# Kernel tuning notes

Hardware: AMD Instinct MI355X
Metric: run time of the kernel (lower is better)

The kernel has to match this reference:

```python
import jax, jax.numpy as jnp
import numpy as np
import math

B, D, H, DK = 24, 64, 8, 8
N, M, CN = 256, 64, 16
VW, VC, CE, WE = 30000, 128, 200, 300

FREQS = jnp.asarray(np.array([10000.0 ** (-i / D) if i % 2 == 0 else -(10000.0 ** (-(i - 1) / D)) for i in range(D)], dtype=np.float32)[:, None])
PHASES = jnp.asarray(np.array([0.0 if i % 2 == 0 else math.pi / 2 for i in range(D)], dtype=np.float32)[:, None])

def _norm(x, eps=1e-6):
    mu = x.mean(-1, keepdims=True)
    var = ((x - mu) ** 2).sum(-1, keepdims=True) / (x.shape[-1] - 1)  # torch std is unbiased
    return (x - mu) / (jnp.sqrt(var) + eps)

def _pos_enc(x):
    pos = jnp.arange(x.shape[-1], dtype=x.dtype)[None, :]
    return jnp.sin(jnp.sin(pos * FREQS + PHASES)) + x  # double sin kept faithful to source

def _conv1d(x, w, groups=1, pad=0, b=None):
    y = jax.lax.conv_general_dilated(x, w, (1,), [(pad, pad)], dimension_numbers=('NCH', 'OIH', 'NCH'), feature_group_count=groups)
    return y if b is None else y + b[None, :, None]

def _dwsep1d(x, dw, pw, db=None, pb=None):
    y = _conv1d(x, dw, groups=x.shape[1], pad=dw.shape[-1] // 2, b=db)
    return _conv1d(y, pw, b=pb)

def _conv2d(x, w, groups=1, pad=0, b=None):
    y = jax.lax.conv_general_dilated(x, w, (1, 1), [(pad, pad), (pad, pad)], dimension_numbers=('NCHW', 'OIHW', 'NCHW'), feature_group_count=groups)
    return y if b is None else y + b[None, :, None, None]

def _highway(x, lw, lb, gw, gb):
    x = x.transpose(0, 2, 1)  # [B,L,D]
    for i in range(lw.shape[0]):
        g = jax.nn.sigmoid(jnp.einsum('bld,od->blo', x, gw[i]) + gb[i])
        nl = jax.nn.relu(jnp.einsum('bld,od->blo', x, lw[i]) + lb[i])
        x = g * nl + (1.0 - g) * x
    return x.transpose(0, 2, 1)

def _embed(ch, wd, e2dw, e2db, e2pw, e2pb, e1dw, e1db, e1pw, e1pb, hlw, hlb, hgw, hgb):
    ch = ch.transpose(0, 3, 1, 2)  # [B,CE,L,CN]
    ch = _conv2d(ch, e2dw, groups=CE, pad=2, b=e2db)
    ch = _conv2d(ch, e2pw, b=e2pb)
    ch = jax.nn.relu(ch).max(axis=3)  # [B,D,L]
    wd = wd.transpose(0, 2, 1)  # [B,WE,L]
    emb = jnp.concatenate([ch, wd], axis=1)
    emb = _dwsep1d(emb, e1dw, e1pw, e1db, e1pb)
    return _highway(emb, hlw, hlb, hgw, hgb)

def _self_att(x, wq, wk, wv, wo):
    Qh = jnp.einsum('hbkd,bdl->hbkl', wq, x)
    Kh = jnp.einsum('hbkd,bdl->hbkl', wk, x)
    Vh = jnp.einsum('hbkd,bdl->hbkl', wv, x)
    scores = jnp.einsum('hbkl,hbkm->hblm', Qh, Kh) / math.sqrt(DK)
    att = jax.nn.softmax(scores, axis=2)  # torch softmax dim=1 over [B,l,m]
    head = jnp.einsum('hbvl,hblm->hbvm', Vh, att)
    head = head.transpose(1, 0, 2, 3).reshape(B, H * DK, x.shape[-1])
    return jnp.einsum('bod,bdl->bol', wo, head)

def _enc_block(x, dw, pw, wq, wk, wv, wo, W):
    out = _pos_enc(x)
    res = out
    for i in range(dw.shape[0]):
        out = jax.nn.relu(_dwsep1d(_norm(out), dw[i], pw[i]))
        out = res + out
        res = out  # dropout is a no-op in this deterministic reference
    out = res + _self_att(_norm(out), wq, wk, wv, wo)
    res = out
    out = jax.nn.relu(jnp.einsum('bod,bdl->bol', W, _norm(out)))
    return res + out

def _cq_att(C, Q, W):
    # S[b,i,j] = W . [Q[:,j]; C[:,i]; Q[:,j]*C[:,i]] -- vectorized trilinear similarity
    wq, wc, wm = W[:, 0, :D], W[:, 0, D:2 * D], W[:, 0, 2 * D:]
    S = (jnp.einsum('bd,bdn->bn', wc, C)[:, :, None]
         + jnp.einsum('bd,bdm->bm', wq, Q)[:, None, :]
         + jnp.einsum('bdn,bdm->bnm', C * wm[:, :, None], Q))
    S1 = jax.nn.softmax(S, axis=2)
    S2 = jax.nn.softmax(S, axis=1)
    A = jnp.einsum('bdm,bnm->bdn', Q, S1)
    X = jnp.einsum('bnm,bkm->bnk', S1, S2)  # S1 @ S2^T
    Bm = jnp.einsum('bdn,bkn->bdk', C, X)   # C @ X^T
    return jnp.concatenate([C, A, C * A, C * Bm], axis=1)

def _pointer(M0, M1, M2, w0, w1):
    Y0 = jnp.einsum('bd,bdn->bn', w0[:, 0], jnp.concatenate([M0, M1], axis=1))
    Y1 = jnp.einsum('bd,bdn->bn', w1[:, 0], jnp.concatenate([M0, M2], axis=1))
    return jax.nn.softmax(Y0, axis=1), jax.nn.softmax(Y1, axis=1)  # exp(log_softmax)

def _qanet(flt, Cwid, Ccid, Qwid, Qcid):
    (word_table, char_table,
     e2dw, e2db, e2pw, e2pb, e1dw, e1db, e1pw, e1pb,
     hlw, hlb, hgw, hgb,
     ce_dw, ce_pw, ce_wq, ce_wk, ce_wv, ce_wo, ce_w,
     qe_dw, qe_pw, qe_wq, qe_wk, qe_wv, qe_wo, qe_w,
     m0_dw, m0_pw, m0_wq, m0_wk, m0_wv, m0_wo, m0_w,
     m1_dw, m1_pw, m1_wq, m1_wk, m1_wv, m1_wo, m1_w,
     m2_dw, m2_pw, m2_wq, m2_wk, m2_wv, m2_wo, m2_w,
     cq_w, rs_dw, rs_pw, p_w0, p_w1) = flt
    emb_p = (e2dw, e2db, e2pw, e2pb, e1dw, e1db, e1pw, e1pb, hlw, hlb, hgw, hgb)
    C = _embed(char_table[Ccid], word_table[Cwid], *emb_p)
    Q = _embed(char_table[Qcid], word_table[Qwid], *emb_p)
    C = _enc_block(C, ce_dw, ce_pw, ce_wq, ce_wk, ce_wv, ce_wo, ce_w)
    Q = _enc_block(Q, qe_dw, qe_pw, qe_wq, qe_wk, qe_wv, qe_wo, qe_w)
    X = _cq_att(C, Q, cq_w)
    X = _dwsep1d(X, rs_dw, rs_pw)
    M0 = X
    for _ in range(7):
        M0 = _enc_block(M0, m0_dw, m0_pw, m0_wq, m0_wk, m0_wv, m0_wo, m0_w)
    M1 = M0
    for _ in range(7):
        M1 = _enc_block(M1, m1_dw, m1_pw, m1_wq, m1_wk, m1_wv, m1_wo, m1_w)
    M2 = M1
    for _ in range(7):
        M2 = _enc_block(M2, m2_dw, m2_pw, m2_wq, m2_wk, m2_wv, m2_wo, m2_w)
    return _pointer(M0, M1, M2, p_w0, p_w1)

def setup_inputs() -> dict:
    key = jax.random.key(0)
    ks = iter(jax.random.split(key, 80))
    rn = lambda shape, s=0.1: jax.random.normal(next(ks), shape, jnp.float32) * s
    inp = {}
    inp['word_table'] = rn((VW, WE), 1.0)
    inp['char_table'] = rn((VC, CE), 1.0)
    inp['e2dw'] = rn((CE, 1, 5, 5)); inp['e2db'] = jnp.zeros((CE,), jnp.float32)
    inp['e2pw'] = rn((D, CE, 1, 1)); inp['e2pb'] = jnp.zeros((D,), jnp.float32)
    inp['e1dw'] = rn((WE + D, 1, 5)); inp['e1db'] = jnp.zeros((WE + D,), jnp.float32)
    inp['e1pw'] = rn((D, WE + D, 1)); inp['e1pb'] = jnp.zeros((D,), jnp.float32)
    inp['hlw'] = rn((2, D, D)); inp['hlb'] = jnp.zeros((2, D), jnp.float32)
    inp['hgw'] = rn((2, D, D)); inp['hgb'] = jnp.zeros((2, D), jnp.float32)
    for p, (cnum, k_) in [('ce', (4, 7)), ('qe', (4, 7)), ('m0', (2, 5)), ('m1', (2, 5)), ('m2', (2, 5))]:
        inp[p + '_dw'] = rn((cnum, D, 1, k_))
        inp[p + '_pw'] = rn((cnum, D, D, 1))
        inp[p + '_wq'] = rn((H, B, DK, D))
        inp[p + '_wk'] = rn((H, B, DK, D))
        inp[p + '_wv'] = rn((H, B, DK, D))
        inp[p + '_wo'] = rn((B, D, D))
        inp[p + '_w'] = rn((B, D, D))
    inp['cq_w'] = rn((B, 1, 3 * D))
    inp['rs_dw'] = rn((4 * D, 1, 5))
    inp['rs_pw'] = rn((D, 4 * D, 1))
    inp['p_w0'] = rn((B, 1, 2 * D))
    inp['p_w1'] = rn((B, 1, 2 * D))
    inp['Cwid'] = jax.random.randint(next(ks), (B, N), 0, VW)
    inp['Ccid'] = jax.random.randint(next(ks), (B, N, CN), 0, VC)
    inp['Qwid'] = jax.random.randint(next(ks), (B, M), 0, VW)
    inp['Qcid'] = jax.random.randint(next(ks), (B, M, CN), 0, VC)
    return inp

def reference(word_table, char_table, e2dw, e2db, e2pw, e2pb, e1dw, e1db, e1pw, e1pb, hlw, hlb, hgw, hgb, ce_dw, ce_pw, ce_wq, ce_wk, ce_wv, ce_wo, ce_w, qe_dw, qe_pw, qe_wq, qe_wk, qe_wv, qe_wo, qe_w, m0_dw, m0_pw, m0_wq, m0_wk, m0_wv, m0_wo, m0_w, m1_dw, m1_pw, m1_wq, m1_wk, m1_wv, m1_wo, m1_w, m2_dw, m2_pw, m2_wq, m2_wk, m2_wv, m2_wo, m2_w, cq_w, rs_dw, rs_pw, p_w0, p_w1, Cwid, Ccid, Qwid, Qcid):
    flt = (word_table, char_table, e2dw, e2db, e2pw, e2pb, e1dw, e1db, e1pw, e1pb, hlw, hlb, hgw, hgb, ce_dw, ce_pw, ce_wq, ce_wk, ce_wv, ce_wo, ce_w, qe_dw, qe_pw, qe_wq, qe_wk, qe_wv, qe_wo, qe_w, m0_dw, m0_pw, m0_wq, m0_wk, m0_wv, m0_wo, m0_w, m1_dw, m1_pw, m1_wq, m1_wk, m1_wv, m1_wo, m1_w, m2_dw, m2_pw, m2_wq, m2_wk, m2_wv, m2_wo, m2_w, cq_w, rs_dw, rs_pw, p_w0, p_w1)
    p0, p1 = _qanet(flt, Cwid, Ccid, Qwid, Qcid)
    return p0, p1
```

## Files before the change

### kernel.cpp

```cpp
#include <hip/hip_runtime.h>
#include <math.h>

constexpr int B = 24, HH = 8;
constexpr int NN = 256, MQ = 64;
constexpr int EC = 364;

#define PI_2 1.5707963267948966f

__device__ __forceinline__ void combine_stats(const float* __restrict__ parts,
                                              int row, int NT, float Lf,
                                              float& mu, float& inv) {
  float s = 0.f, q = 0.f;
  for (int t = 0; t < NT; ++t) {
    s += parts[((size_t)row * 4 + t) * 2];
    q += parts[((size_t)row * 4 + t) * 2 + 1];
  }
  mu = s / Lf;
  float var = (q - s * mu) / (Lf - 1.f);
  if (var < 0.f) var = 0.f;
  inv = 1.f / (sqrtf(var) + 1e-6f);
}

__global__ void k_prep(float* __restrict__ tab,
                       const float* __restrict__ e2pw, const float* __restrict__ e1pw,
                       const float* __restrict__ hlw, const float* __restrict__ hgw,
                       const float* __restrict__ e2dw,
                       float* __restrict__ pwT, float* __restrict__ e1pwT,
                       float* __restrict__ hlwT, float* __restrict__ hgwT,
                       float* __restrict__ dwT) {
  int blk = blockIdx.x;
  if (blk < 64) {
    int d = blk, l = threadIdx.x;
    float fr = ((d & 1) == 0) ? powf(10000.f, -(float)d / 64.f)
                              : -powf(10000.f, -(float)(d - 1) / 64.f);
    float ph = (d & 1) ? PI_2 : 0.f;
    tab[d * 256 + l] = sinf(sinf((float)l * fr + ph));
    return;
  }
  int i = (blk - 64) * 256 + threadIdx.x;
  if (i < 12800) {
    int ce = i >> 6, o = i & 63;
    pwT[i] = e2pw[o * 200 + ce];
    return;
  }
  i -= 12800;
  if (i < 23296) {
    int c = i >> 6, o = i & 63;
    e1pwT[i] = e1pw[o * EC + c];
    return;
  }
  i -= 23296;
  if (i < 8192) {
    int layer = i >> 12, rem = i & 4095;
    int d = rem >> 6, o = rem & 63;
    hlwT[i] = hlw[layer * 4096 + o * 64 + d];
    return;
  }
  i -= 8192;
  if (i < 8192) {
    int layer = i >> 12, rem = i & 4095;
    int d = rem >> 6, o = rem & 63;
    hgwT[i] = hgw[layer * 4096 + o * 64 + d];
    return;
  }
  i -= 8192;
  if (i < 5000) {
    int t = i / 200, ce = i % 200;
    dwT[i] = e2dw[ce * 25 + t];
  }
}

template<bool COPY>
__global__ void k_posadd_stats(float* __restrict__ XC, const float* __restrict__ srcC,
                               float* __restrict__ XQ, const float* __restrict__ tab,
                               float* __restrict__ partsC, float* __restrict__ partsQ) {
  int which = blockIdx.y;
  float* X = which ? XQ : XC;
  float* parts = which ? partsQ : partsC;
  int L = which ? 64 : 256;
  int row = blockIdx.x * 4 + (threadIdx.x >> 6);
  int lane = threadIdx.x & 63;
  int d = row & 63;
  float* xr = X + (size_t)row * L;
  const float* sr = (COPY && !which) ? (srcC + (size_t)row * L) : xr;
  int NT = L >> 6;
  for (int t = 0; t < NT; ++t) {
    int l = t * 64 + lane;
    float v = sr[l] + tab[d * 256 + l];
    xr[l] = v;
    float s = v, q = v * v;
#pragma unroll
    for (int o = 32; o > 0; o >>= 1) { s += __shfl_xor(s, o); q += __shfl_xor(q, o); }
    if (lane == 0) {
      parts[((size_t)row * 4 + t) * 2] = s;
      parts[((size_t)row * 4 + t) * 2 + 1] = q;
    }
  }
}

template<int K>
__global__ __launch_bounds__(512) void k_fconv(
    const float* __restrict__ XiC, float* __restrict__ XoC,
    const float* __restrict__ XiQ, float* __restrict__ XoQ,
    const float* __restrict__ dwC, const float* __restrict__ pwC,
    const float* __restrict__ dwQ, const float* __restrict__ pwQ,
    const float* __restrict__ pinC, float* __restrict__ poutC,
    const float* __restrict__ pinQ, float* __restrict__ poutQ) {
  constexpr int H = K / 2, SW = 64 + 2 * H;
  __shared__ float smu[64], sinv[64];
  __shared__ float sN[64 * SW];
  __shared__ float sD[64 * 65];
  __shared__ __align__(16) float sWt[4096];
  int b = blockIdx.x, t = blockIdx.y;
  const float *Xin, *dw, *pw, *pin; float *Xout, *pout; int L, tile;
  if (t < 4) { Xin = XiC; Xout = XoC; dw = dwC; pw = pwC; pin = pinC; pout = poutC; L = 256; tile = t; }
  else       { Xin = XiQ; Xout = XoQ; dw = dwQ; pw = pwQ; pin = pinQ; pout = poutQ; L = 64;  tile = 0; }
  int lt = tile * 64;
  int tid = threadIdx.x;
  int NT = L >> 6;
  if (tid < 64) combine_stats(pin, b * 64 + tid, NT, (float)L, smu[tid], sinv[tid]);
  for (int i = tid; i < 1024; i += 512)
    ((float4*)sWt)[i] = ((const float4*)pw)[i];
  const float* Xb = Xin + (size_t)b * 64 * L;
  int l = tid & 63, og = tid >> 6;
  float rres[8];
#pragma unroll
  for (int j = 0; j < 8; ++j)
    rres[j] = Xb[(size_t)(og * 8 + j) * L + lt + l];
  __syncthreads();
  for (int i = tid; i < 64 * SW; i += 512) {
    int c = i / SW, jj = i % SW;
    int gl = lt + jj - H;
    sN[i] = (gl >= 0 && gl < L) ? (Xb[(size_t)c * L + gl] - smu[c]) * sinv[c] : 0.f;
  }
  __syncthreads();
  for (int i = tid; i < 4096; i += 512) {
    int c = i >> 6, ll = i & 63;
    float acc = 0.f;
#pragma unroll
    for (int k = 0; k < K; ++k) acc += sN[c * SW + ll + k] * dw[c * K + k];
    sD[c * 65 + ll] = acc;
  }
  __syncthreads();
  float acc[8];
#pragma unroll
  for (int j = 0; j < 8; ++j) acc[j] = 0.f;
  for (int c = 0; c < 64; ++c) {
    float av = sD[c * 65 + l];
#pragma unroll
    for (int j = 0; j < 8; ++j) acc[j] += sWt[(og * 8 + j) * 64 + c] * av;
  }
  __syncthreads();
  float* Ob = Xout + (size_t)b * 64 * L;
#pragma unroll
  for (int j = 0; j < 8; ++j) {
    int o = og * 8 + j;
    float v = rres[j] + fmaxf(acc[j], 0.f);
    Ob[(size_t)o * L + lt + l] = v;
    sD[o * 65 + l] = v;
  }
  __syncthreads();
  if (tid < 64) {
    int o = tid;
    float s = 0.f, q = 0.f;
    for (int l2 = 0; l2 < 64; ++l2) { float v = sD[o * 65 + l2]; s += v; q += v * v; }
    pout[((size_t)(b * 64 + o) * 4 + tile) * 2] = s;
    pout[((size_t)(b * 64 + o) * 4 + tile) * 2 + 1] = q;
  }
}

template<bool NORM, bool RELU, bool STATS, bool ADDTAB>
__global__ __launch_bounds__(512) void k_matmul2(
    const float* __restrict__ AC, const float* __restrict__ WC,
    const float* __restrict__ resC, float* __restrict__ outC2,
    const float* __restrict__ pinC, float* __restrict__ poutC,
    const float* __restrict__ AQ, const float* __restrict__ WQ,
    const float* __restrict__ resQ, float* __restrict__ outQ2,
    const float* __restrict__ pinQ, float* __restrict__ poutQ,
    const float* __restrict__ tab) {
  __shared__ float sA[64 * 65];
  __shared__ __align__(16) float sW[4096];
  __shared__ float smu[64], sinv[64];
  int b = blockIdx.x, t = blockIdx.y;
  const float *A, *W, *res, *pin; float *outp, *pout; int L, tile;
  if (t < 4) { A = AC; W = WC; res = resC; outp = outC2; pin = pinC; pout = poutC; L = 256; tile = t; }
  else       { A = AQ; W = WQ; res = resQ; outp = outQ2; pin = pinQ; pout = poutQ; L = 64;  tile = 0; }
  int lt = tile * 64;
  int tid = threadIdx.x;
  int NT = L >> 6;
  if (NORM && tid < 64) combine_stats(pin, b * 64 + tid, NT, (float)L, smu[tid], sinv[tid]);
  const float* Wb = W + (size_t)b * 4096;
  for (int i = tid; i < 1024; i += 512)
    ((float4*)sW)[i] = ((const float4*)Wb)[i];
  int l = tid & 63, og = tid >> 6;
  float rres[8], rtab[8];
#pragma unroll
  for (int j = 0; j < 8; ++j) {
    int o = og * 8 + j;
    rres[j] = res[((size_t)b * 64 + o) * L + lt + l];
    if (ADDTAB) rtab[j] = tab[o * 256 + lt + l];
  }
  if (NORM) __syncthreads();
  const float* Ab = A + (size_t)b * 64 * L;
  for (int i = tid; i < 1024; i += 512) {
    int c = i >> 4, lq = (i & 15) * 4;
    float4 v = *(const float4*)(Ab + (size_t)c * L + lt + lq);
    if (NORM) {
      float mu = smu[c], iv = sinv[c];
      v.x = (v.x - mu) * iv; v.y = (v.y - mu) * iv;
      v.z = (v.z - mu) * iv; v.w = (v.w - mu) * iv;
    }
    sA[c * 65 + lq] = v.x; sA[c * 65 + lq + 1] = v.y;
    sA[c * 65 + lq + 2] = v.z; sA[c * 65 + lq + 3] = v.w;
  }
  __syncthreads();
  float acc[8];
#pragma unroll
  for (int j = 0; j < 8; ++j) acc[j] = 0.f;
  for (int c = 0; c < 64; ++c) {
    float av = sA[c * 65 + l];
#pragma unroll
    for (int j = 0; j < 8; ++j) acc[j] += sW[(og * 8 + j) * 64 + c] * av;
  }
  if (STATS) __syncthreads();
#pragma unroll
  for (int j = 0; j < 8; ++j) {
    int o = og * 8 + j;
    float v = acc[j];
    if (RELU) v = fmaxf(v, 0.f);
    v += rres[j];
    if (ADDTAB) v += rtab[j];
    outp[((size_t)b * 64 + o) * L + lt + l] = v;
    if (STATS) sA[o * 65 + l] = v;
  }
  if (STATS) {
    __syncthreads();
    if (tid < 64) {
      int o = tid;
      float s = 0.f, q = 0.f;
      for (int l2 = 0; l2 < 64; ++l2) { float v = sA[o * 65 + l2]; s += v; q += v * v; }
      pout[((size_t)(b * 64 + o) * 4 + tile) * 2] = s;
      pout[((size_t)(b * 64 + o) * 4 + tile) * 2 + 1] = q;
    }
  }
}

__global__ __launch_bounds__(256) void k_resize(
    const float* __restrict__ Xcat, const float* __restrict__ dw,
    const float* __restrict__ pw, float* __restrict__ out) {
  __shared__ float sA[64 * 64];
  int b = blockIdx.x, lt = blockIdx.y * 64;
  int l = threadIdx.x & 63, og = threadIdx.x >> 6;
  float acc[16];
#pragma unroll
  for (int j = 0; j < 16; ++j) acc[j] = 0.f;
  for (int c0 = 0; c0 < 256; c0 += 64) {
    __syncthreads();
    for (int i = threadIdx.x; i < 4096; i += 256) {
      int c = (i >> 6) + c0, ll = (i & 63) + lt;
      const float* xr = Xcat + ((size_t)b * 256 + c) * 256;
      float a = 0.f;
#pragma unroll
      for (int k = 0; k < 5; ++k) {
        int p = ll + k - 2;
        if (p >= 0 && p < 256) a += xr[p] * dw[c * 5 + k];
      }
      sA[i] = a;
    }
    __syncthreads();
    for (int c = 0; c < 64; ++c) {
      float av = sA[c * 64 + l];
#pragma unroll
      for (int j = 0; j < 16; ++j)
        acc[j] += pw[(size_t)(og * 16 + j) * 256 + c0 + c] * av;
    }
  }
#pragma unroll
  for (int j = 0; j < 16; ++j)
    out[((size_t)b * 64 + og * 16 + j) * 256 + lt + l] = acc[j];
}

__global__ __launch_bounds__(512) void k_att(
    const float* __restrict__ XC, const float* __restrict__ partsC,
    const float* __restrict__ wqC, const float* __restrict__ wkC,
    const float* __restrict__ wvC, float* __restrict__ hcC,
    const float* __restrict__ XQ, const float* __restrict__ partsQ,
    const float* __restrict__ wqQ, const float* __restrict__ wkQ,
    const float* __restrict__ wvQ, float* __restrict__ hcQ) {
  int h = blockIdx.x, b2 = blockIdx.y;
  const float *X, *parts, *wq, *wk, *wv; float* hc; int L, b;
  if (b2 < B) { X = XC; parts = partsC; wq = wqC; wk = wkC; wv = wvC; hc = hcC; L = 256; b = b2; }
  else        { X = XQ; parts = partsQ; wq = wqQ; wk = wkQ; wv = wvQ; hc = hcQ; L = 64;  b = b2 - B; }
  __shared__ float smu[64], sinv[64];
  __shared__ float sX[64 * 65];
  __shared__ float sQ[2048], sK8[2048], sV[2048];
  __shared__ float swq[512], swk[512], swv[512];
  int tid = threadIdx.x;
  int NT = L >> 6;
  if (tid < 64) combine_stats(parts, b * 64 + tid, NT, (float)L, smu[tid], sinv[tid]);
  size_t woff = (size_t)(h * B + b) * 512;
  swq[tid] = wq[woff + tid];
  swk[tid] = wk[woff + tid];
  swv[tid] = wv[woff + tid];
  __syncthreads();
  const float* Xb = X + (size_t)b * 64 * L;
  for (int lt = 0; lt < L; lt += 64) {
    for (int i = tid; i < 4096; i += 512) {
      int d = i >> 6, l = i & 63;
      sX[d * 65 + l] = (Xb[(size_t)d * L + lt + l] - smu[d]) * sinv[d];
    }
    __syncthreads();
    {
      int k = tid >> 6, l = tid & 63;
      float aq = 0.f, ak = 0.f, av = 0.f;
      for (int d = 0; d < 64; ++d) {
        float x = sX[d * 65 + l];
        aq += swq[k * 64 + d] * x;
        ak += swk[k * 64 + d] * x;
        av += swv[k * 64 + d] * x;
      }
      sQ[k * L + lt + l] = aq; sK8[k * L + lt + l] = ak; sV[k * L + lt + l] = av;
    }
    __syncthreads();
  }
  const float scale = 0.35355339059327373f;
  int m = tid & 255, half = tid >> 8;
  int L2 = L >> 1;
  float mx = -1e30f, sum = 0.f, acc[8];
#pragma unroll
  for (int v = 0; v < 8; ++v) acc[v] = 0.f;
  if (m < L) {
    float kc[8];
#pragma unroll
    for (int k = 0; k < 8; ++k) kc[k] = sK8[k * L + m];
    int l0 = half * L2, l1 = l0 + L2;
    for (int l = l0; l < l1; ++l) {
      float s = 0.f;
#pragma unroll
      for (int k = 0; k < 8; ++k) s += sQ[k * L + l] * kc[k];
      s *= scale;
      if (s <= mx) {
        float p = __expf(s - mx);
        sum += p;
#pragma unroll
        for (int v = 0; v < 8; ++v) acc[v] += p * sV[v * L + l];
      } else {
        float corr = __expf(mx - s);
        sum = sum * corr + 1.f;
#pragma unroll
        for (int v = 0; v < 8; ++v) acc[v] = acc[v] * corr + sV[v * L + l];
        mx = s;
      }
    }
  }
  swq[tid] = mx;
  swk[tid] = sum;
  float* pacc = sX;
#pragma unroll
  for (int v = 0; v < 8; ++v) pacc[tid * 8 + v] = acc[v];
  __syncthreads();
  if (half == 0 && m < L) {
    float m0 = swq[m], m1 = swq[256 + m];
    float mT = fmaxf(m0, m1);
    float c0 = __expf(m0 - mT), c1 = __expf(m1 - mT);
    float s = swk[m] * c0 + swk[256 + m] * c1;
    float is = 1.f / s;
#pragma unroll
    for (int v = 0; v < 8; ++v) {
      float a = pacc[m * 8 + v] * c0 + pacc[(256 + m) * 8 + v] * c1;
      hc[((size_t)b * 64 + h * 8 + v) * L + m] = a * is;
    }
  }
}

__global__ __launch_bounds__(256) void k_charembed(
    const int* __restrict__ cidC, const int* __restrict__ cidQ,
    const float* __restrict__ ctab, const float* __restrict__ dwT,
    const float* __restrict__ db, const float* __restrict__ pwT,
    const float* __restrict__ pb,
    float* __restrict__ outC, float* __restrict__ outQ) {
  int nx = blockIdx.x, b = blockIdx.y;
  const int* cid; float* out; int Ln, n;
  if (nx < NN) { cid = cidC; out = outC; Ln = NN; n = nx; }
  else         { cid = cidQ; out = outQ; Ln = MQ; n = nx - NN; }
  __shared__ float dwo[16 * 200];
  __shared__ int sid[5][16];
  __shared__ float red[256];
  int tid = threadIdx.x;
  if (tid < 80) {
    int kn = tid / 16, cn = tid % 16;
    int nn = n + kn - 2;
    sid[kn][cn] = (nn >= 0 && nn < Ln) ? cid[((size_t)b * Ln + nn) * 16 + cn] : -1;
  }
  __syncthreads();
  for (int i = tid; i < 16 * 200; i += 256) {
    int cn = i / 200, ce = i % 200;
    float r[25];
#pragma unroll
    for (int kn = 0; kn < 5; ++kn) {
#pragma unroll
      for (int kc = 0; kc < 5; ++kc) {
        int cc = cn + kc - 2;
        int id = (cc >= 0 && cc < 16) ? sid[kn][cc] : -1;
        r[kn * 5 + kc] = (id >= 0) ? ctab[(size_t)id * 200 + ce] : 0.f;
      }
    }
    float acc = db[ce];
#pragma unroll
    for (int t = 0; t < 25; ++t) acc += r[t] * dwT[t * 200 + ce];
    dwo[cn * 200 + ce] = acc;
  }
  __syncthreads();
  int o = tid & 63, q = tid >> 6;
  float acc4[4];
#pragma unroll
  for (int k = 0; k < 4; ++k) acc4[k] = pb[o];
  for (int c0 = 0; c0 < 200; c0 += 8) {
    float w8[8];
#pragma unroll
    for (int j = 0; j < 8; ++j) w8[j] = pwT[(c0 + j) * 64 + o];
#pragma unroll
    for (int k = 0; k < 4; ++k) {
      const float* dr = dwo + (q + k * 4) * 200 + c0;
#pragma unroll
      for (int j = 0; j < 8; ++j) acc4[k] += w8[j] * dr[j];
    }
  }
  float mx = -1e30f;
#pragma unroll
  for (int k = 0; k < 4; ++k) mx = fmaxf(mx, acc4[k]);
  red[tid] = mx;
  __syncthreads();
  if (q == 0) {
    mx = fmaxf(fmaxf(red[o], red[64 + o]), fmaxf(red[128 + o], red[192 + o]));
    out[((size_t)b * 64 + o) * Ln + n] = fmaxf(mx, 0.f);
  }
}

__global__ void k_embhw(const float* __restrict__ chxC, const float* __restrict__ chxQ,
                        const int* __restrict__ widC, const int* __restrict__ widQ,
                        const float* __restrict__ wtab, const float* __restrict__ dw,
                        const float* __restrict__ db, const float* __restrict__ pwT,
                        const float* __restrict__ pb,
                        const float* __restrict__ lwT, const float* __restrict__ lb,
                        const float* __restrict__ gwT, const float* __restrict__ gb,
                        float* __restrict__ outC, float* __restrict__ outQ) {
  int nx = blockIdx.x, b = blockIdx.y;
  const float* chx; const int* wid; float* out; int Ln, n;
  if (nx < NN) { chx = chxC; wid = widC; out = outC; Ln = NN; n = nx; }
  else         { chx = chxQ; wid = widQ; out = outQ; Ln = MQ; n = nx - NN; }
  __shared__ float dwc[EC];
  __shared__ int sw[5];
  __shared__ float x[64], xn[64];
  int tid = threadIdx.x;
  if (tid < 5) {
    int nn = n + tid - 2;
    sw[tid] = (nn >= 0 && nn < Ln) ? wid[(size_t)b * Ln + nn] : -1;
  }
  __syncthreads();
  for (int ch = tid; ch < EC; ch += 64) {
    float r[5];
#pragma unroll
    for (int k = 0; k < 5; ++k) {
      int nn = n + k - 2;
      float v = 0.f;
      if (nn >= 0 && nn < Ln) {
        if (ch < 64) v = chx[((size_t)b * 64 + ch) * Ln + nn];
        else v = wtab[(size_t)sw[k] * 300 + (ch - 64)];
      }
      r[k] = v;
    }
    float acc = db[ch];
#pragma unroll
    for (int k = 0; k < 5; ++k) acc += r[k] * dw[ch * 5 + k];
    dwc[ch] = acc;
  }
  __syncthreads();
  int o = tid;
  float acc = pb[o];
  for (int c0 = 0; c0 < EC; c0 += 4) {
    float w4[4];
#pragma unroll
    for (int j = 0; j < 4; ++j) w4[j] = pwT[(c0 + j) * 64 + o];
#pragma unroll
    for (int j = 0; j < 4; ++j) acc += w4[j] * dwc[c0 + j];
  }
  x[o] = acc;
  __syncthreads();
  for (int layer = 0; layer < 2; ++layer) {
    const float* lwr = lwT + layer * 4096;
    const float* gwr = gwT + layer * 4096;
    float gl = gb[layer * 64 + o], nl = lb[layer * 64 + o];
    for (int d0 = 0; d0 < 64; d0 += 8) {
      float g8[8], l8[8];
#pragma unroll
      for (int j = 0; j < 8; ++j) { g8[j] = gwr[(d0 + j) * 64 + o]; l8[j] = lwr[(d0 + j) * 64 + o]; }
#pragma unroll
      for (int j = 0; j < 8; ++j) { gl += g8[j] * x[d0 + j]; nl += l8[j] * x[d0 + j]; }
    }
    float g = 1.f / (1.f + __expf(-gl));
    float r = fmaxf(nl, 0.f);
    xn[o] = g * r + (1.f - g) * x[o];
    __syncthreads();
    x[o] = xn[o];
    __syncthreads();
  }
  out[((size_t)b * 64 + o) * Ln + n] = x[o];
}

__global__ __launch_bounds__(256) void k_cqS(const float* __restrict__ C,
                                             const float* __restrict__ Q,
                                             const float* __restrict__ w,
                                             float* __restrict__ S,
                                             float* __restrict__ rmax,
                                             float* __restrict__ rsum) {
  int b = blockIdx.x, nt = blockIdx.y * 64;
  __shared__ float sQ[4096], sC[4096], ct[64], qt[64], swb[192];
  const float* Cb = C + (size_t)b * 64 * 256;
  const float* Qb = Q + (size_t)b * 4096;
  const float* wb = w + (size_t)b * 192;
  if (threadIdx.x < 192) swb[threadIdx.x] = wb[threadIdx.x];
  for (int i = threadIdx.x; i < 4096; i += 256) {
    int d = i >> 6, m = i & 63;
    sQ[i] = Qb[d * 64 + m];
    sC[i] = Cb[d * 256 + nt + m];
  }
  __syncthreads();
  if (threadIdx.x < 64) {
    int j = threadIdx.x;
    float a = 0.f, c2 = 0.f;
    for (int d = 0; d < 64; ++d) {
      a += swb[64 + d] * sC[d * 64 + j];
      c2 += swb[d] * sQ[d * 64 + j];
    }
    ct[j] = a; qt[j] = c2;
  }
  __syncthreads();
  int m = threadIdx.x & 63, wv = threadIdx.x >> 6;
  for (int it = 0; it < 16; ++it) {
    int nl = wv + it * 4;
    float acc = ct[nl] + qt[m];
    for (int d = 0; d < 64; ++d)
      acc += sC[d * 64 + nl] * swb[128 + d] * sQ[d * 64 + m];
    S[((size_t)b * 256 + nt + nl) * 64 + m] = acc;
    float mx = acc;
#pragma unroll
    for (int o = 32; o > 0; o >>= 1) mx = fmaxf(mx, __shfl_xor(mx, o));
    float p = __expf(acc - mx);
#pragma unroll
    for (int o = 32; o > 0; o >>= 1) p += __shfl_xor(p, o);
    if (m == 0) { rmax[b * 256 + nt + nl] = mx; rsum[b * 256 + nt + nl] = p; }
  }
}

__global__ void k_cqcol(const float* __restrict__ S, float* __restrict__ cmax,
                        float* __restrict__ csum) {
  int b = blockIdx.x, m = threadIdx.x;
  const float* Sb = S + (size_t)b * 256 * 64;
  float mx = -1e30f;
  for (int n = 0; n < 256; ++n) mx = fmaxf(mx, Sb[n * 64 + m]);
  float s = 0.f;
  for (int n = 0; n < 256; ++n) s += __expf(Sb[n * 64 + m] - mx);
  cmax[b * 64 + m] = mx; csum[b * 64 + m] = s;
}

__global__ __launch_bounds__(256) void k_cqA_CS2(
    const float* __restrict__ C, const float* __restrict__ Q,
    const float* __restrict__ S, const float* __restrict__ rmax,
    const float* __restrict__ rsum, const float* __restrict__ cmax,
    const float* __restrict__ csum, float* __restrict__ Xcat,
    float* __restrict__ CS2) {
  __shared__ float sh[8256];
  int b = blockIdx.x, t = blockIdx.y;
  int tid = threadIdx.x;
  if (t < 4) {
    float* sQ = sh; float* sP = sh + 4096;
    int nt = t * 64;
    const float* Qb = Q + (size_t)b * 4096;
    for (int i = tid; i < 4096; i += 256) sQ[i] = Qb[i];
    for (int i = tid; i < 4096; i += 256) {
      int nl = i >> 6, m = i & 63;
      int n = nt + nl;
      sP[nl * 65 + m] = __expf(S[((size_t)b * 256 + n) * 64 + m] - rmax[b * 256 + n]) / rsum[b * 256 + n];
    }
    __syncthreads();
    int nl = tid & 63, dg = tid >> 6;
    int n = nt + nl;
    for (int j = 0; j < 16; ++j) {
      int d = dg * 16 + j;
      float acc = 0.f;
      for (int m = 0; m < 64; ++m) acc += sQ[d * 64 + m] * sP[nl * 65 + m];
      float cv = C[((size_t)b * 64 + d) * 256 + n];
      Xcat[((size_t)b * 256 + d) * 256 + n] = cv;
      Xcat[((size_t)b * 256 + 64 + d) * 256 + n] = acc;
      Xcat[((size_t)b * 256 + 128 + d) * 256 + n] = cv * acc;
    }
  } else {
    float* sP = sh; float* sC = sh + 4096;
    int m = tid & 63, dg = tid >> 6;
    float acc[16];
#pragma unroll
    for (int j = 0; j < 16; ++j) acc[j] = 0.f;
    for (int nt = 0; nt < 4; ++nt) {
      __syncthreads();
      for (int i = tid; i < 4096; i += 256) {
        int nl = i >> 6, mm = i & 63;
        int n = nt * 64 + nl;
        sP[i] = __expf(S[((size_t)b * 256 + n) * 64 + mm] - cmax[b * 64 + mm]) / csum[b * 64 + mm];
        int d = i >> 6, nn = i & 63;
        sC[i] = C[((size_t)b * 64 + d) * 256 + nt * 64 + nn];
      }
      __syncthreads();
      for (int nl = 0; nl < 64; ++nl) {
        float p = sP[nl * 64 + m];
#pragma unroll
        for (int j = 0; j < 16; ++j) acc[j] += sC[(dg * 16 + j) * 64 + nl] * p;
      }
    }
    for (int j = 0; j < 16; ++j)
      CS2[((size_t)b * 64 + dg * 16 + j) * 64 + m] = acc[j];
  }
}

__global__ __launch_bounds__(256) void k_cqBm(
    const float* __restrict__ C, const float* __restrict__ CS2,
    const float* __restrict__ S, const float* __restrict__ rmax,
    const float* __restrict__ rsum, float* __restrict__ Xcat) {
  int b = blockIdx.x, kt = blockIdx.y * 64;
  __shared__ float sW[4096];
  __shared__ float sP[64 * 65];
  for (int i = threadIdx.x; i < 4096; i += 256) sW[i] = CS2[(size_t)b * 4096 + i];
  for (int i = threadIdx.x; i < 4096; i += 256) {
    int kl = i >> 6, m = i & 63;
    int k = kt + kl;
    sP[kl * 65 + m] = __expf(S[((size_t)b * 256 + k) * 64 + m] - rmax[b * 256 + k]) / rsum[b * 256 + k];
  }
  __syncthreads();
  int kl = threadIdx.x & 63, dg = threadIdx.x >> 6;
  int k = kt + kl;
  for (int j = 0; j < 16; ++j) {
    int d = dg * 16 + j;
    float acc = 0.f;
    for (int m = 0; m < 64; ++m) acc += sW[d * 64 + m] * sP[kl * 65 + m];
    float cv = C[((size_t)b * 64 + d) * 256 + k];
    Xcat[((size_t)b * 256 + 192 + d) * 256 + k] = cv * acc;
  }
}

__global__ void k_pointer2(const float* __restrict__ M0, const float* __restrict__ M1,
                           const float* __restrict__ M2, const float* __restrict__ w0,
                           const float* __restrict__ w1, float* __restrict__ out) {
  int b = blockIdx.x, sel = blockIdx.y, n = threadIdx.x;
  const float* wb = (sel ? w1 : w0) + b * 128;
  const float* Mb = sel ? M2 : M1;
  float y = 0.f;
  for (int d = 0; d < 64; ++d) {
    y += wb[d] * M0[((size_t)b * 64 + d) * 256 + n];
    y += wb[64 + d] * Mb[((size_t)b * 64 + d) * 256 + n];
  }
  __shared__ float wred[4], wsum[4];
  int lane = n & 63, wid = n >> 6;
  float mx = y;
#pragma unroll
  for (int o = 32; o > 0; o >>= 1) mx = fmaxf(mx, __shfl_xor(mx, o));
  if (lane == 0) wred[wid] = mx;
  __syncthreads();
  mx = fmaxf(fmaxf(wred[0], wred[1]), fmaxf(wred[2], wred[3]));
  float e = __expf(y - mx);
  float s = e;
#pragma unroll
  for (int o = 32; o > 0; o >>= 1) s += __shfl_xor(s, o);
  if (lane == 0) wsum[wid] = s;
  __syncthreads();
  s = wsum[0] + wsum[1] + wsum[2] + wsum[3];
  out[sel * 6144 + b * 256 + n] = e / s;
}

extern "C" void kernel_launch(void* const* d_in, const int* in_sizes, int n_in,
                              void* d_out, int out_size, void* d_ws, size_t ws_size,
                              hipStream_t stream) {
  const float* word_table = (const float*)d_in[0];
  const float* char_table = (const float*)d_in[1];
  const float* e2dw = (const float*)d_in[2];
  const float* e2db = (const float*)d_in[3];
  const float* e2pw = (const float*)d_in[4];
  const float* e2pb = (const float*)d_in[5];
  const float* e1dw = (const float*)d_in[6];
  const float* e1db = (const float*)d_in[7];
  const float* e1pw = (const float*)d_in[8];
  const float* e1pb = (const float*)d_in[9];
  const float* hlw = (const float*)d_in[10];
  const float* hlb = (const float*)d_in[11];
  const float* hgw = (const float*)d_in[12];
  const float* hgb = (const float*)d_in[13];
  const float *enc_dw[5], *enc_pw[5], *enc_wq[5], *enc_wk[5], *enc_wv[5], *enc_wo[5], *enc_w[5];
  for (int p = 0; p < 5; ++p) {
    enc_dw[p] = (const float*)d_in[14 + 7 * p + 0];
    enc_pw[p] = (const float*)d_in[14 + 7 * p + 1];
    enc_wq[p] = (const float*)d_in[14 + 7 * p + 2];
    enc_wk[p] = (const float*)d_in[14 + 7 * p + 3];
    enc_wv[p] = (const float*)d_in[14 + 7 * p + 4];
    enc_wo[p] = (const float*)d_in[14 + 7 * p + 5];
    enc_w[p]  = (const float*)d_in[14 + 7 * p + 6];
  }
  const float* cq_w  = (const float*)d_in[49];
  const float* rs_dw = (const float*)d_in[50];
  const float* rs_pw = (const float*)d_in[51];
  const float* p_w0  = (const float*)d_in[52];
  const float* p_w1  = (const float*)d_in[53];
  const int* Cwid = (const int*)d_in[54];
  const int* Ccid = (const int*)d_in[55];
  const int* Qwid = (const int*)d_in[56];
  const int* Qcid = (const int*)d_in[57];
  float* out = (float*)d_out;

  float* ws = (float*)d_ws;
  float* postab = ws;
  float* U    = ws + 16384;
  float* Xcat = ws + 409600;
  float* CX   = ws + 1982464;
  float* Sb   = ws + 2375680;
  float* QX   = ws + 2768896;
  float* CS2  = ws + 2867200;
  float* rmax = ws + 2965504;
  float* rsum = ws + 2971648;
  float* cmax = ws + 2977792;
  float* csum = ws + 2979328;
  float* P0   = ws + 2980864;
  float* P1   = ws + 2993152;
  float* pwT  = ws + 3005440;
  float* e1pwT= ws + 3018240;
  float* hlwT = ws + 3041536;
  float* hgwT = ws + 3049728;
  float* dwT  = ws + 3057920;
  float* P0Q  = ws + 3062920;
  float* P1Q  = ws + 3075208;
  float* UQ   = ws + 3087496;
  float* M0 = CX; float* M1 = Sb; float* M2 = Xcat;
  float* E1C = Xcat;
  float* E1Q = Xcat + 393216;
  (void)out_size; (void)in_sizes; (void)n_in; (void)ws_size;

  auto run_enc = [&](float* X, const float* src, int p, int reps) {
    if (src)
      hipLaunchKernelGGL((k_posadd_stats<true>), dim3(384, 1), dim3(256), 0, stream,
                         X, src, (float*)nullptr, postab, P0, (float*)nullptr);
    else
      hipLaunchKernelGGL((k_posadd_stats<false>), dim3(384, 1), dim3(256), 0, stream,
                         X, (const float*)nullptr, (float*)nullptr, postab, P0, (float*)nullptr);
    for (int rep = 0; rep < reps; ++rep) {
      float* pin = P0; float* pout = P1;
      float* Xi = X; float* Xo = U;
      for (int i = 0; i < 2; ++i) {
        hipLaunchKernelGGL((k_fconv<5>), dim3(B, 4), dim3(512), 0, stream,
                           (const float*)Xi, Xo, (const float*)nullptr, (float*)nullptr,
                           enc_dw[p] + i * 64 * 5, enc_pw[p] + (size_t)i * 4096,
                           (const float*)nullptr, (const float*)nullptr,
                           pin, pout, (const float*)nullptr, (float*)nullptr);
        { float* t = pin; pin = pout; pout = t; }
        { float* t = Xi; Xi = Xo; Xo = t; }
      }
      k_att<<<dim3(HH, B), 512, 0, stream>>>(X, pin, enc_wq[p], enc_wk[p], enc_wv[p], U,
                                             (const float*)nullptr, (const float*)nullptr,
                                             (const float*)nullptr, (const float*)nullptr,
                                             (const float*)nullptr, (float*)nullptr);
      hipLaunchKernelGGL((k_matmul2<false, false, true, false>), dim3(B, 4), dim3(512), 0, stream,
                         (const float*)U, enc_wo[p], (const float*)X, X, (const float*)nullptr, pout,
                         (const float*)nullptr, (const float*)nullptr, (const float*)nullptr,
                         (float*)nullptr, (const float*)nullptr, (float*)nullptr,
                         (const float*)nullptr);
      if (rep + 1 < reps)
        hipLaunchKernelGGL((k_matmul2<true, true, true, true>), dim3(B, 4), dim3(512), 0, stream,
                           (const float*)X, enc_w[p], (const float*)X, X, pout, P0,
                           (const float*)nullptr, (const float*)nullptr, (const float*)nullptr,
                           (float*)nullptr, (const float*)nullptr, (float*)nullptr,
                           (const float*)postab);
      else
        hipLaunchKernelGGL((k_matmul2<true, true, false, false>), dim3(B, 4), dim3(512), 0, stream,
                           (const float*)X, enc_w[p], (const float*)X, X, pout, (float*)nullptr,
                           (const float*)nullptr, (const float*)nullptr, (const float*)nullptr,
                           (float*)nullptr, (const float*)nullptr, (float*)nullptr,
                           (const float*)nullptr);
    }
  };

  k_prep<<<289, 256, 0, stream>>>(postab, e2pw, e1pw, hlw, hgw, e2dw,
                                  pwT, e1pwT, hlwT, hgwT, dwT);
  k_charembed<<<dim3(NN + MQ, B), 256, 0, stream>>>(Ccid, Qcid, char_table, dwT, e2db, pwT, e2pb, E1C, E1Q);
  k_embhw<<<dim3(NN + MQ, B), 64, 0, stream>>>(E1C, E1Q, Cwid, Qwid, word_table, e1dw, e1db,
                                               e1pwT, e1pb, hlwT, hlb, hgwT, hgb, CX, QX);
  {
    hipLaunchKernelGGL((k_posadd_stats<false>), dim3(384, 2), dim3(256), 0, stream,
                       CX, (const float*)nullptr, QX, postab, P0, P0Q);
    float *pinC = P0, *poutC = P1, *pinQ = P0Q, *poutQ = P1Q;
    float *XiC = CX, *XoC = U, *XiQ = QX, *XoQ = UQ;
    for (int i = 0; i < 4; ++i) {
      hipLaunchKernelGGL((k_fconv<7>), dim3(B, 5), dim3(512), 0, stream,
                         (const float*)XiC, XoC, (const float*)XiQ, XoQ,
                         enc_dw[0] + i * 64 * 7, enc_pw[0] + (size_t)i * 4096,
                         enc_dw[1] + i * 64 * 7, enc_pw[1] + (size_t)i * 4096,
                         pinC, poutC, pinQ, poutQ);
      { float* t = pinC; pinC = poutC; poutC = t; }
      { float* t = pinQ; pinQ = poutQ; poutQ = t; }
      { float* t = XiC; XiC = XoC; XoC = t; }
      { float* t = XiQ; XiQ = XoQ; XoQ = t; }
    }
    k_att<<<dim3(HH, 2 * B), 512, 0, stream>>>(CX, pinC, enc_wq[0], enc_wk[0], enc_wv[0], U,
                                               QX, pinQ, enc_wq[1], enc_wk[1], enc_wv[1], UQ);
    hipLaunchKernelGGL((k_matmul2<false, false, true, false>), dim3(B, 5), dim3(512), 0, stream,
                       (const float*)U, enc_wo[0], (const float*)CX, CX, (const float*)nullptr, poutC,
                       (const float*)UQ, enc_wo[1], (const float*)QX, QX, (const float*)nullptr, poutQ,
                       (const float*)nullptr);
    hipLaunchKernelGGL((k_matmul2<true, true, false, false>), dim3(B, 5), dim3(512), 0, stream,
                       (const float*)CX, enc_w[0], (const float*)CX, CX, poutC, (float*)nullptr,
                       (const float*)QX, enc_w[1], (const float*)QX, QX, poutQ, (float*)nullptr,
                       (const float*)nullptr);
  }
  k_cqS<<<dim3(B, 4), 256, 0, stream>>>(CX, QX, cq_w, Sb, rmax, rsum);
  k_cqcol<<<B, 64, 0, stream>>>(Sb, cmax, csum);
  k_cqA_CS2<<<dim3(B, 5), 256, 0, stream>>>(CX, QX, Sb, rmax, rsum, cmax, csum, Xcat, CS2);
  k_cqBm<<<dim3(B, 4), 256, 0, stream>>>(CX, CS2, Sb, rmax, rsum, Xcat);
  k_resize<<<dim3(B, 4), 256, 0, stream>>>(Xcat, rs_dw, rs_pw, M0);
  run_enc(M0, nullptr, 2, 7);
  run_enc(M1, M0, 3, 7);
  run_enc(M2, M1, 4, 7);
  k_pointer2<<<dim3(B, 2), 256, 0, stream>>>(M0, M1, M2, p_w0, p_w1, out);
}
```

Before: 2.431 ms.

## Fuse model-encoder posadd/stats into producers and use 1024-thread conv/matmul blocks

Removes the separate k_posadd_stats launches before each model encoder pass. The resize kernel now adds the positional table and writes row statistics itself, and the last FFN matmul of each encoder writes both its output and the next encoder's table-added input with stats (DUAL mode). Separately, the fconv and matmul2 kernels go from 512 to 1024 threads with 4 outputs per thread instead of 8. This raises parallelism within each block but halves per-thread register reuse of the shared-memory activation loads.

```diff
diff --git a/kernel.cpp b/kernel.cpp
--- a/kernel.cpp
+++ b/kernel.cpp
@@ -70,9 +70,8 @@
   }
 }
 
-template<bool COPY>
-__global__ void k_posadd_stats(float* __restrict__ XC, const float* __restrict__ srcC,
-                               float* __restrict__ XQ, const float* __restrict__ tab,
+__global__ void k_posadd_stats(float* __restrict__ XC, float* __restrict__ XQ,
+                               const float* __restrict__ tab,
                                float* __restrict__ partsC, float* __restrict__ partsQ) {
   int which = blockIdx.y;
   float* X = which ? XQ : XC;
@@ -82,11 +81,10 @@
   int lane = threadIdx.x & 63;
   int d = row & 63;
   float* xr = X + (size_t)row * L;
-  const float* sr = (COPY && !which) ? (srcC + (size_t)row * L) : xr;
   int NT = L >> 6;
   for (int t = 0; t < NT; ++t) {
     int l = t * 64 + lane;
-    float v = sr[l] + tab[d * 256 + l];
+    float v = xr[l] + tab[d * 256 + l];
     xr[l] = v;
     float s = v, q = v * v;
 #pragma unroll
@@ -99,7 +97,7 @@
 }
 
 template<int K>
-__global__ __launch_bounds__(512) void k_fconv(
+__global__ __launch_bounds__(1024) void k_fconv(
     const float* __restrict__ XiC, float* __restrict__ XoC,
     const float* __restrict__ XiQ, float* __restrict__ XoQ,
     const float* __restrict__ dwC, const float* __restrict__ pwC,
@@ -119,22 +117,22 @@
   int tid = threadIdx.x;
   int NT = L >> 6;
   if (tid < 64) combine_stats(pin, b * 64 + tid, NT, (float)L, smu[tid], sinv[tid]);
-  for (int i = tid; i < 1024; i += 512)
+  for (int i = tid; i < 1024; i += 1024)
     ((float4*)sWt)[i] = ((const float4*)pw)[i];
   const float* Xb = Xin + (size_t)b * 64 * L;
   int l = tid & 63, og = tid >> 6;
-  float rres[8];
-#pragma unroll
-  for (int j = 0; j < 8; ++j)
-    rres[j] = Xb[(size_t)(og * 8 + j) * L + lt + l];
-  __syncthreads();
-  for (int i = tid; i < 64 * SW; i += 512) {
+  float rres[4];
+#pragma unroll
+  for (int j = 0; j < 4; ++j)
+    rres[j] = Xb[(size_t)(og * 4 + j) * L + lt + l];
+  __syncthreads();
+  for (int i = tid; i < 64 * SW; i += 1024) {
     int c = i / SW, jj = i % SW;
     int gl = lt + jj - H;
     sN[i] = (gl >= 0 && gl < L) ? (Xb[(size_t)c * L + gl] - smu[c]) * sinv[c] : 0.f;
   }
   __syncthreads();
-  for (int i = tid; i < 4096; i += 512) {
+  for (int i = tid; i < 4096; i += 1024) {
     int c = i >> 6, ll = i & 63;
     float acc = 0.f;
 #pragma unroll
@@ -142,19 +140,19 @@
     sD[c * 65 + ll] = acc;
   }
   __syncthreads();
-  float acc[8];
-#pragma unroll
-  for (int j = 0; j < 8; ++j) acc[j] = 0.f;
+  float acc[4];
+#pragma unroll
+  for (int j = 0; j < 4; ++j) acc[j] = 0.f;
   for (int c = 0; c < 64; ++c) {
     float av = sD[c * 65 + l];
 #pragma unroll
-    for (int j = 0; j < 8; ++j) acc[j] += sWt[(og * 8 + j) * 64 + c] * av;
+    for (int j = 0; j < 4; ++j) acc[j] += sWt[(og * 4 + j) * 64 + c] * av;
   }
   __syncthreads();
   float* Ob = Xout + (size_t)b * 64 * L;
 #pragma unroll
-  for (int j = 0; j < 8; ++j) {
-    int o = og * 8 + j;
+  for (int j = 0; j < 4; ++j) {
+    int o = og * 4 + j;
     float v = rres[j] + fmaxf(acc[j], 0.f);
     Ob[(size_t)o * L + lt + l] = v;
     sD[o * 65 + l] = v;
@@ -169,15 +167,15 @@
   }
 }
 
-template<bool NORM, bool RELU, bool STATS, bool ADDTAB>
-__global__ __launch_bounds__(512) void k_matmul2(
+template<bool NORM, bool RELU, bool STATS, bool ADDTAB, bool DUAL>
+__global__ __launch_bounds__(1024) void k_matmul2(
     const float* __restrict__ AC, const float* __restrict__ WC,
     const float* __restrict__ resC, float* __restrict__ outC2,
     const float* __restrict__ pinC, float* __restrict__ poutC,
     const float* __restrict__ AQ, const float* __restrict__ WQ,
     const float* __restrict__ resQ, float* __restrict__ outQ2,
     const float* __restrict__ pinQ, float* __restrict__ poutQ,
-    const float* __restrict__ tab) {
+    float* __restrict__ outNextC, const float* __restrict__ tab) {
   __shared__ float sA[64 * 65];
   __shared__ __align__(16) float sW[4096];
   __shared__ float smu[64], sinv[64];
@@ -190,19 +188,19 @@
   int NT = L >> 6;
   if (NORM && tid < 64) combine_stats(pin, b * 64 + tid, NT, (float)L, smu[tid], sinv[tid]);
   const float* Wb = W + (size_t)b * 4096;
-  for (int i = tid; i < 1024; i += 512)
+  for (int i = tid; i < 1024; i += 1024)
     ((float4*)sW)[i] = ((const float4*)Wb)[i];
   int l = tid & 63, og = tid >> 6;
-  float rres[8], rtab[8];
-#pragma unroll
-  for (int j = 0; j < 8; ++j) {
-    int o = og * 8 + j;
+  float rres[4], rtab[4];
+#pragma unroll
+  for (int j = 0; j < 4; ++j) {
+    int o = og * 4 + j;
     rres[j] = res[((size_t)b * 64 + o) * L + lt + l];
-    if (ADDTAB) rtab[j] = tab[o * 256 + lt + l];
+    if (ADDTAB || DUAL) rtab[j] = tab[o * 256 + lt + l];
   }
   if (NORM) __syncthreads();
   const float* Ab = A + (size_t)b * 64 * L;
-  for (int i = tid; i < 1024; i += 512) {
+  for (int i = tid; i < 1024; i += 1024) {
     int c = i >> 4, lq = (i & 15) * 4;
     float4 v = *(const float4*)(Ab + (size_t)c * L + lt + lq);
     if (NORM) {
@@ -214,24 +212,31 @@
     sA[c * 65 + lq + 2] = v.z; sA[c * 65 + lq + 3] = v.w;
   }
   __syncthreads();
-  float acc[8];
-#pragma unroll
-  for (int j = 0; j < 8; ++j) acc[j] = 0.f;
+  float acc[4];
+#pragma unroll
+  for (int j = 0; j < 4; ++j) acc[j] = 0.f;
   for (int c = 0; c < 64; ++c) {
     float av = sA[c * 65 + l];
 #pragma unroll
-    for (int j = 0; j < 8; ++j) acc[j] += sW[(og * 8 + j) * 64 + c] * av;
+    for (int j = 0; j < 4; ++j) acc[j] += sW[(og * 4 + j) * 64 + c] * av;
   }
   if (STATS) __syncthreads();
 #pragma unroll
-  for (int j = 0; j < 8; ++j) {
-    int o = og * 8 + j;
+  for (int j = 0; j < 4; ++j) {
+    int o = og * 4 + j;
     float v = acc[j];
     if (RELU) v = fmaxf(v, 0.f);
     v += rres[j];
-    if (ADDTAB) v += rtab[j];
-    outp[((size_t)b * 64 + o) * L + lt + l] = v;
-    if (STATS) sA[o * 65 + l] = v;
+    if (DUAL) {
+      float vn = v + rtab[j];
+      outp[((size_t)b * 64 + o) * L + lt + l] = v;
+      outNextC[((size_t)b * 64 + o) * L + lt + l] = vn;
+      if (STATS) sA[o * 65 + l] = vn;
+    } else {
+      if (ADDTAB) v += rtab[j];
+      outp[((size_t)b * 64 + o) * L + lt + l] = v;
+      if (STATS) sA[o * 65 + l] = v;
+    }
   }
   if (STATS) {
     __syncthreads();
@@ -247,8 +252,9 @@
 
 __global__ __launch_bounds__(256) void k_resize(
     const float* __restrict__ Xcat, const float* __restrict__ dw,
-    const float* __restrict__ pw, float* __restrict__ out) {
-  __shared__ float sA[64 * 64];
+    const float* __restrict__ pw, const float* __restrict__ tab,
+    float* __restrict__ out, float* __restrict__ parts) {
+  __shared__ float sA[64 * 65];
   int b = blockIdx.x, lt = blockIdx.y * 64;
   int l = threadIdx.x & 63, og = threadIdx.x >> 6;
   float acc[16];
@@ -265,19 +271,32 @@
         int p = ll + k - 2;
         if (p >= 0 && p < 256) a += xr[p] * dw[c * 5 + k];
       }
-      sA[i] = a;
+      sA[(i >> 6) * 65 + (i & 63)] = a;
     }
     __syncthreads();
     for (int c = 0; c < 64; ++c) {
-      float av = sA[c * 64 + l];
+      float av = sA[c * 65 + l];
 #pragma unroll
       for (int j = 0; j < 16; ++j)
         acc[j] += pw[(size_t)(og * 16 + j) * 256 + c0 + c] * av;
     }
   }
-#pragma unroll
-  for (int j = 0; j < 16; ++j)
-    out[((size_t)b * 64 + og * 16 + j) * 256 + lt + l] = acc[j];
+  __syncthreads();
+#pragma unroll
+  for (int j = 0; j < 16; ++j) {
+    int o = og * 16 + j;
+    float v = acc[j] + tab[o * 256 + lt + l];
+    out[((size_t)b * 64 + o) * 256 + lt + l] = v;
+    sA[o * 65 + l] = v;
+  }
+  __syncthreads();
+  if (threadIdx.x < 64) {
+    int o = threadIdx.x;
+    float s = 0.f, q = 0.f;
+    for (int l2 = 0; l2 < 64; ++l2) { float v = sA[o * 65 + l2]; s += v; q += v * v; }
+    parts[((size_t)(b * 64 + o) * 4 + blockIdx.y) * 2] = s;
+    parts[((size_t)(b * 64 + o) * 4 + blockIdx.y) * 2 + 1] = q;
+  }
 }
 
 __global__ __launch_bounds__(512) void k_att(
@@ -741,18 +760,12 @@
   float* E1Q = Xcat + 393216;
   (void)out_size; (void)in_sizes; (void)n_in; (void)ws_size;
 
-  auto run_enc = [&](float* X, const float* src, int p, int reps) {
-    if (src)
-      hipLaunchKernelGGL((k_posadd_stats<true>), dim3(384, 1), dim3(256), 0, stream,
-                         X, src, (float*)nullptr, postab, P0, (float*)nullptr);
-    else
-      hipLaunchKernelGGL((k_posadd_stats<false>), dim3(384, 1), dim3(256), 0, stream,
-                         X, (const float*)nullptr, (float*)nullptr, postab, P0, (float*)nullptr);
-    for (int rep = 0; rep < reps; ++rep) {
+  auto run_enc = [&](float* X, float* Xnext, int p) {
+    for (int rep = 0; rep < 7; ++rep) {
       float* pin = P0; float* pout = P1;
       float* Xi = X; float* Xo = U;
       for (int i = 0; i < 2; ++i) {
-        hipLaunchKernelGGL((k_fconv<5>), dim3(B, 4), dim3(512), 0, stream,
+        hipLaunchKernelGGL((k_fconv<5>), dim3(B, 4), dim3(1024), 0, stream,
                            (const float*)Xi, Xo, (const float*)nullptr, (float*)nullptr,
                            enc_dw[p] + i * 64 * 5, enc_pw[p] + (size_t)i * 4096,
                            (const float*)nullptr, (const float*)nullptr,
@@ -764,23 +777,29 @@
                                              (const float*)nullptr, (const float*)nullptr,
                                              (const float*)nullptr, (const float*)nullptr,
                                              (const float*)nullptr, (float*)nullptr);
-      hipLaunchKernelGGL((k_matmul2<false, false, true, false>), dim3(B, 4), dim3(512), 0, stream,
+      hipLaunchKernelGGL((k_matmul2<false, false, true, false, false>), dim3(B, 4), dim3(1024), 0, stream,
                          (const float*)U, enc_wo[p], (const float*)X, X, (const float*)nullptr, pout,
                          (const float*)nullptr, (const float*)nullptr, (const float*)nullptr,
                          (float*)nullptr, (const float*)nullptr, (float*)nullptr,
-                         (const float*)nullptr);
-      if (rep + 1 < reps)
-        hipLaunchKernelGGL((k_matmul2<true, true, true, true>), dim3(B, 4), dim3(512), 0, stream,
+                         (float*)nullptr, (const float*)nullptr);
+      if (rep < 6)
+        hipLaunchKernelGGL((k_matmul2<true, true, true, true, false>), dim3(B, 4), dim3(1024), 0, stream,
                            (const float*)X, enc_w[p], (const float*)X, X, pout, P0,
                            (const float*)nullptr, (const float*)nullptr, (const float*)nullptr,
                            (float*)nullptr, (const float*)nullptr, (float*)nullptr,
-                           (const float*)postab);
+                           (float*)nullptr, (const float*)postab);
+      else if (Xnext)
+        hipLaunchKernelGGL((k_matmul2<true, true, true, false, true>), dim3(B, 4), dim3(1024), 0, stream,
+                           (const float*)X, enc_w[p], (const float*)X, X, pout, P0,
+                           (const float*)nullptr, (const float*)nullptr, (const float*)nullptr,
+                           (float*)nullptr, (const float*)nullptr, (float*)nullptr,
+                           Xnext, (const float*)postab);
       else
-        hipLaunchKernelGGL((k_matmul2<true, true, false, false>), dim3(B, 4), dim3(512), 0, stream,
+        hipLaunchKernelGGL((k_matmul2<true, true, false, false, false>), dim3(B, 4), dim3(1024), 0, stream,
                            (const float*)X, enc_w[p], (const float*)X, X, pout, (float*)nullptr,
                            (const float*)nullptr, (const float*)nullptr, (const float*)nullptr,
                            (float*)nullptr, (const float*)nullptr, (float*)nullptr,
-                           (const float*)nullptr);
+                           (float*)nullptr, (const float*)nullptr);
     }
   };
 
@@ -790,12 +809,11 @@
   k_embhw<<<dim3(NN + MQ, B), 64, 0, stream>>>(E1C, E1Q, Cwid, Qwid, word_table, e1dw, e1db,
                                                e1pwT, e1pb, hlwT, hlb, hgwT, hgb, CX, QX);
   {
-    hipLaunchKernelGGL((k_posadd_stats<false>), dim3(384, 2), dim3(256), 0, stream,
-                       CX, (const float*)nullptr, QX, postab, P0, P0Q);
+    k_posadd_stats<<<dim3(384, 2), 256, 0, stream>>>(CX, QX, postab, P0, P0Q);
     float *pinC = P0, *poutC = P1, *pinQ = P0Q, *poutQ = P1Q;
     float *XiC = CX, *XoC = U, *XiQ = QX, *XoQ = UQ;
     for (int i = 0; i < 4; ++i) {
-      hipLaunchKernelGGL((k_fconv<7>), dim3(B, 5), dim3(512), 0, stream,
+      hipLaunchKernelGGL((k_fconv<7>), dim3(B, 5), dim3(1024), 0, stream,
                          (const float*)XiC, XoC, (const float*)XiQ, XoQ,
                          enc_dw[0] + i * 64 * 7, enc_pw[0] + (size_t)i * 4096,
                          enc_dw[1] + i * 64 * 7, enc_pw[1] + (size_t)i * 4096,
@@ -807,22 +825,22 @@
     }
     k_att<<<dim3(HH, 2 * B), 512, 0, stream>>>(CX, pinC, enc_wq[0], enc_wk[0], enc_wv[0], U,
                                                QX, pinQ, enc_wq[1], enc_wk[1], enc_wv[1], UQ);
-    hipLaunchKernelGGL((k_matmul2<false, false, true, false>), dim3(B, 5), dim3(512), 0, stream,
+    hipLaunchKernelGGL((k_matmul2<false, false, true, false, false>), dim3(B, 5), dim3(1024), 0, stream,
                        (const float*)U, enc_wo[0], (const float*)CX, CX, (const float*)nullptr, poutC,
                        (const float*)UQ, enc_wo[1], (const float*)QX, QX, (const float*)nullptr, poutQ,
-                       (const float*)nullptr);
-    hipLaunchKernelGGL((k_matmul2<true, true, false, false>), dim3(B, 5), dim3(512), 0, stream,
+                       (float*)nullptr, (const float*)nullptr);
+    hipLaunchKernelGGL((k_matmul2<true, true, false, false, false>), dim3(B, 5), dim3(1024), 0, stream,
                        (const float*)CX, enc_w[0], (const float*)CX, CX, poutC, (float*)nullptr,
                        (const float*)QX, enc_w[1], (const float*)QX, QX, poutQ, (float*)nullptr,
-                       (const float*)nullptr);
+                       (float*)nullptr, (const float*)nullptr);
   }
   k_cqS<<<dim3(B, 4), 256, 0, stream>>>(CX, QX, cq_w, Sb, rmax, rsum);
   k_cqcol<<<B, 64, 0, stream>>>(Sb, cmax, csum);
   k_cqA_CS2<<<dim3(B, 5), 256, 0, stream>>>(CX, QX, Sb, rmax, rsum, cmax, csum, Xcat, CS2);
   k_cqBm<<<dim3(B, 4), 256, 0, stream>>>(CX, CS2, Sb, rmax, rsum, Xcat);
-  k_resize<<<dim3(B, 4), 256, 0, stream>>>(Xcat, rs_dw, rs_pw, M0);
-  run_enc(M0, nullptr, 2, 7);
-  run_enc(M1, M0, 3, 7);
-  run_enc(M2, M1, 4, 7);
+  k_resize<<<dim3(B, 4), 256, 0, stream>>>(Xcat, rs_dw, rs_pw, postab, M0, P0);
+  run_enc(M0, M1, 2);
+  run_enc(M1, M2, 3);
+  run_enc(M2, nullptr, 4);
   k_pointer2<<<dim3(B, 2), 256, 0, stream>>>(M0, M1, M2, p_w0, p_w1, out);
 }
```

Measured after the change: 2.230 ms. -8.3%, faster.
